# Optimization experiments

Hardware: AMD Instinct MI355X
Metric: run time of the kernel (lower is better)

## Reference

```python
import jax, jax.numpy as jnp
import numpy as np

HIDDEN = 64
EXPAND = 2
INNER = HIDDEN * EXPAND
KSIZE = 4


def setup_inputs() -> dict:
    key = jax.random.key(0)
    ks = jax.random.split(key, 12)
    s = 0.02
    inp = {
        "x": jax.random.normal(ks[0], (4, 64, 1024, HIDDEN), jnp.float32),
        "w_in": jax.random.normal(ks[1], (HIDDEN, 2 * INNER), jnp.float32) * s,
        "b_in": jnp.zeros((2 * INNER,), jnp.float32),
        "w_conv": jax.random.normal(ks[2], (INNER, 1, KSIZE), jnp.float32) * s,  # depthwise: [C,1,K]
        "b_conv": jnp.zeros((INNER,), jnp.float32),
        "w_delta": jax.random.normal(ks[3], (INNER, INNER), jnp.float32) * s,
        "b_delta": jnp.zeros((INNER,), jnp.float32),
        "w_si": jax.random.normal(ks[4], (INNER, INNER), jnp.float32) * s,
        "b_si": jnp.zeros((INNER,), jnp.float32),
        "w_so": jax.random.normal(ks[5], (INNER, INNER), jnp.float32) * s,
        "b_so": jnp.zeros((INNER,), jnp.float32),
        "a_log": jnp.zeros((INNER,), jnp.float32),   # nn.Parameter(torch.zeros)
        "d_skip": jnp.ones((INNER,), jnp.float32),   # nn.Parameter(torch.ones)
        "w_out": jax.random.normal(ks[6], (INNER, HIDDEN), jnp.float32) * s,
        "b_out": jnp.zeros((HIDDEN,), jnp.float32),
    }
    return inp


def _forward(x, w_in, b_in, w_conv, b_conv, w_delta, b_delta, w_si, b_si,
             w_so, b_so, a_log, d_skip, w_out, b_out):
    B, T, N, H = x.shape
    # [B,T,N,H] -> [B*N, T, H]
    xr = jnp.transpose(x, (0, 2, 1, 3)).reshape(B * N, T, H)
    proj = xr @ w_in + b_in                      # [BN, T, 2*inner]
    signal, gate = jnp.split(proj, 2, axis=-1)
    # causal depthwise conv1d (pad left K-1, crop to T == torch pad=K-1 then [:T])
    sc = jnp.transpose(signal, (0, 2, 1))        # [BN, inner, T]
    sc = jax.lax.conv_general_dilated(
        sc, w_conv, window_strides=(1,), padding=[(KSIZE - 1, 0)],
        dimension_numbers=("NCH", "OIH", "NCH"), feature_group_count=INNER)
    sc = sc + b_conv[None, :, None]
    signal = jax.nn.silu(jnp.transpose(sc, (0, 2, 1)))  # [BN, T, inner]
    # selective scan
    delta = jax.nn.softplus(signal @ w_delta + b_delta)
    s_in = jnp.tanh(signal @ w_si + b_si)
    s_out = jnp.tanh(signal @ w_so + b_so)
    a = -jax.nn.softplus(a_log)                  # [inner]
    decay = jnp.exp(delta * a)                   # [BN, T, inner]

    def step(state, xs):
        dec_t, si_t, so_t, sg_t = xs
        state = dec_t * state + si_t * sg_t
        return state, so_t * state + d_skip * sg_t

    # time-major for scan: [T, BN, inner]
    tm = lambda t: jnp.transpose(t, (1, 0, 2))
    init = jnp.zeros((B * N, INNER), x.dtype)
    _, hidden = jax.lax.scan(step, init, (tm(decay), tm(s_in), tm(s_out), tm(signal)))
    hidden = jnp.transpose(hidden, (1, 0, 2))    # [BN, T, inner]
    hidden = hidden * jax.nn.sigmoid(gate)
    out = hidden @ w_out + b_out                 # [BN, T, H]
    return jnp.transpose(out.reshape(B, N, T, H), (0, 2, 1, 3))


def reference(x, w_in, b_in, w_conv, b_conv, w_delta, b_delta, w_si, b_si,
              w_so, b_so, a_log, d_skip, w_out, b_out):
    return _forward(x, w_in, b_in, w_conv, b_conv, w_delta, b_delta, w_si, b_si,
                    w_so, b_so, a_log, d_skip, w_out, b_out)
```

## Files before the change

kernel.cpp:

```cpp
#include <hip/hip_runtime.h>
#include <math.h>


typedef __bf16 bf16x8 __attribute__((ext_vector_type(8)));
typedef float f32x4 __attribute__((ext_vector_type(4)));

#define LOG2E 1.44269504088896f

#define WIN_E 0
#define WD_E 16384
#define WSI_E 32768
#define WSO_E 49152
#define WOT_E 65536
#define WQ_END 73728
#define AS_BYTE (WQ_END * 2)

__device__ inline float sig_poly(float x) {
  float t = x * x;
  float u = fmaf(t, 1.f / 480.f, -1.f / 48.f);
  u = fmaf(t, u, 0.25f);
  return fmaf(x, u, 0.5f);
}
__device__ inline float tanh_poly(float z) {
  float t = z * z;
  return z * fmaf(t, fmaf(t, 2.f / 15.f, -1.f / 3.f), 1.f);
}

__device__ inline int frag_off(int col, int k, int nct) {
  int ks = k >> 5, lgk = (k >> 3) & 3, j = k & 7;
  return ((ks * nct + (col >> 4)) * 64 + ((col & 15) + (lgk << 4))) * 8 + j;
}

__global__ __launch_bounds__(256) void prep_kernel(
    const float* __restrict__ w_in, const float* __restrict__ w_delta,
    const float* __restrict__ w_si, const float* __restrict__ w_so,
    const float* __restrict__ w_out, const float* __restrict__ a_log,
    __bf16* __restrict__ wq, float* __restrict__ a_s) {
  int i = blockIdx.x * 256 + threadIdx.x;
  if (i < 16384) {
    int col = i & 255, k = i >> 8;
    wq[WIN_E + frag_off(col, k, 16)] = (__bf16)w_in[k * 256 + col];
  } else if (i < 32768) {
    int j = i - 16384, col = j & 127, k = j >> 7;
    wq[WD_E + frag_off(col, k, 8)] = (__bf16)w_delta[k * 128 + col];
  } else if (i < 49152) {
    int j = i - 32768, col = j & 127, k = j >> 7;
    wq[WSI_E + frag_off(col, k, 8)] = (__bf16)w_si[k * 128 + col];
  } else if (i < 65536) {
    int j = i - 49152, col = j & 127, k = j >> 7;
    wq[WSO_E + frag_off(col, k, 8)] = (__bf16)w_so[k * 128 + col];
  } else if (i < 73728) {
    int j = i - 65536, col = j & 63, k = j >> 6;
    wq[WOT_E + frag_off(col, k, 4)] = (__bf16)w_out[k * 64 + col];
  } else if (i < 73856) {
    int c = i - 73728;
    a_s[c] = -log1pf(__expf(a_log[c]));
  }
}

__global__ __launch_bounds__(256, 3) void mamba_main(
    const float* __restrict__ x, const float* __restrict__ b_in,
    const float* __restrict__ w_conv, const float* __restrict__ b_conv,
    const float* __restrict__ b_delta, const float* __restrict__ b_si,
    const float* __restrict__ b_so, const float* __restrict__ d_skip,
    const float* __restrict__ b_out, const __bf16* __restrict__ wqb,
    const float* __restrict__ a_s, float* __restrict__ out) {
  __shared__ __bf16 XS[32 * 72];
  __shared__ __bf16 DH[32 * 136];
  __shared__ __bf16 HG[32 * 136];

  const int tid = threadIdx.x;
  const int lane = tid & 63;
  const int wave = tid >> 6;
  const int lr = lane & 15;
  const int lg = lane >> 4;
  const int lk = lg << 3;
  const int bb = blockIdx.x >> 10;
  const int nn = blockIdx.x & 1023;

  float bsig[2], bgat[2], bdl[2], aC[2], aH[2], aQ[2], bsi[2], bso[2], dskv[2], cbc[2];
  float cw0[2], cw1[2], cw2[2], cw3[2];
#pragma unroll
  for (int ct = 0; ct < 2; ++ct) {
    int sc = wave * 32 + ct * 16 + lr;
    bsig[ct] = b_in[sc];
    bgat[ct] = b_in[128 + sc];
    bdl[ct] = b_delta[sc];
    float a = a_s[sc];
    aC[ct] = a;
    aH[ct] = 0.5f * LOG2E * a;
    aQ[ct] = 0.125f * LOG2E * a;
    bsi[ct] = b_si[sc];
    bso[ct] = b_so[sc];
    dskv[ct] = d_skip[sc];
    cw0[ct] = w_conv[sc * 4 + 0];
    cw1[ct] = w_conv[sc * 4 + 1];
    cw2[ct] = w_conv[sc * 4 + 2];
    cw3[ct] = w_conv[sc * 4 + 3];
    cbc[ct] = b_conv[sc];
  }
  const float bout = b_out[wave * 16 + lr];

  float car1[2] = {0.f, 0.f}, car2[2] = {0.f, 0.f}, car3[2] = {0.f, 0.f};
  float C[2] = {0.f, 0.f};
  float sgv[2][2][4];
  float sigg[2][2][4];

  const int xtr = tid >> 3, xc0 = (tid & 7) * 8;
  {
    const float* xp = x + (((size_t)bb * 64 + xtr) * 1024 + nn) * 64 + xc0;
    float4 v0 = *(const float4*)xp;
    float4 v1 = *(const float4*)(xp + 4);
    bf16x8 pk;
    pk[0] = (__bf16)v0.x; pk[1] = (__bf16)v0.y; pk[2] = (__bf16)v0.z; pk[3] = (__bf16)v0.w;
    pk[4] = (__bf16)v1.x; pk[5] = (__bf16)v1.y; pk[6] = (__bf16)v1.z; pk[7] = (__bf16)v1.w;
    *(bf16x8*)(XS + xtr * 72 + xc0) = pk;
  }
  __syncthreads();

#pragma unroll
  for (int ch = 0; ch < 2; ++ch) {
    const int cbs[4] = {2 * wave, 2 * wave + 1, 8 + 2 * wave, 9 + 2 * wave};
    bf16x8 bw[4][2];
#pragma unroll
    for (int ct = 0; ct < 4; ++ct)
#pragma unroll
      for (int ks = 0; ks < 2; ++ks)
        bw[ct][ks] = *(const bf16x8*)(wqb + WIN_E + (((ks << 4) + cbs[ct]) * 64 + lane) * 8);
    float4 xv0, xv1;
    if (ch == 0) {
      const float* xp = x + (((size_t)bb * 64 + 32 + xtr) * 1024 + nn) * 64 + xc0;
      xv0 = *(const float4*)xp;
      xv1 = *(const float4*)(xp + 4);
    }
    bf16x8 ax[2][2];
#pragma unroll
    for (int mt = 0; mt < 2; ++mt)
#pragma unroll
      for (int ks = 0; ks < 2; ++ks)
        ax[mt][ks] = *(const bf16x8*)(XS + (mt * 16 + lr) * 72 + ks * 32 + lk);
    f32x4 acc[2][4];
    const f32x4 z = {0.f, 0.f, 0.f, 0.f};
#pragma unroll
    for (int mt = 0; mt < 2; ++mt)
#pragma unroll
      for (int ct = 0; ct < 4; ++ct) acc[mt][ct] = z;
#pragma unroll
    for (int ks = 0; ks < 2; ++ks)
#pragma unroll
      for (int ct = 0; ct < 4; ++ct)
#pragma unroll
        for (int mt = 0; mt < 2; ++mt)
          acc[mt][ct] = __builtin_amdgcn_mfma_f32_16x16x32_bf16(ax[mt][ks], bw[ct][ks],
                                                                acc[mt][ct], 0, 0, 0);
#pragma unroll
    for (int ct = 0; ct < 2; ++ct)
#pragma unroll
      for (int mt = 0; mt < 2; ++mt)
#pragma unroll
        for (int r = 0; r < 4; ++r)
          sigg[ct][mt][r] = sig_poly(acc[mt][ct + 2][r] + bgat[ct]);
#pragma unroll
    for (int ct = 0; ct < 2; ++ct) {
      int col = wave * 32 + ct * 16 + lr;
      float s0 = acc[0][ct][0] + bsig[ct], s1 = acc[0][ct][1] + bsig[ct];
      float s2 = acc[0][ct][2] + bsig[ct], s3 = acc[0][ct][3] + bsig[ct];
      float t0 = acc[1][ct][0] + bsig[ct], t1 = acc[1][ct][1] + bsig[ct];
      float t2 = acc[1][ct][2] + bsig[ct], t3 = acc[1][ct][3] + bsig[ct];
      float a3 = __shfl_up(s3, 16), a2 = __shfl_up(s2, 16), a1 = __shfl_up(s1, 16);
      float p1 = lg ? a3 : car1[ct];
      float p2 = lg ? a2 : car2[ct];
      float p3 = lg ? a1 : car3[ct];
      float b3 = __shfl_up(t3, 16), b2 = __shfl_up(t2, 16), b1 = __shfl_up(t1, 16);
      float q15 = __shfl(s3, lr + 48), q14 = __shfl(s2, lr + 48), q13 = __shfl(s1, lr + 48);
      float e1 = lg ? b3 : q15;
      float e2 = lg ? b2 : q14;
      float e3 = lg ? b1 : q13;
      car1[ct] = __shfl(t3, lr + 48);
      car2[ct] = __shfl(t2, lr + 48);
      car3[ct] = __shfl(t1, lr + 48);
      float cv[4], dv[4];
      cv[0] = fmaf(cw0[ct], p3, fmaf(cw1[ct], p2, fmaf(cw2[ct], p1, fmaf(cw3[ct], s0, cbc[ct]))));
      cv[1] = fmaf(cw0[ct], p2, fmaf(cw1[ct], p1, fmaf(cw2[ct], s0, fmaf(cw3[ct], s1, cbc[ct]))));
      cv[2] = fmaf(cw0[ct], p1, fmaf(cw1[ct], s0, fmaf(cw2[ct], s1, fmaf(cw3[ct], s2, cbc[ct]))));
      cv[3] = fmaf(cw0[ct], s0, fmaf(cw1[ct], s1, fmaf(cw2[ct], s2, fmaf(cw3[ct], s3, cbc[ct]))));
      dv[0] = fmaf(cw0[ct], e3, fmaf(cw1[ct], e2, fmaf(cw2[ct], e1, fmaf(cw3[ct], t0, cbc[ct]))));
      dv[1] = fmaf(cw0[ct], e2, fmaf(cw1[ct], e1, fmaf(cw2[ct], t0, fmaf(cw3[ct], t1, cbc[ct]))));
      dv[2] = fmaf(cw0[ct], e1, fmaf(cw1[ct], t0, fmaf(cw2[ct], t1, fmaf(cw3[ct], t2, cbc[ct]))));
      dv[3] = fmaf(cw0[ct], t0, fmaf(cw1[ct], t1, fmaf(cw2[ct], t2, fmaf(cw3[ct], t3, cbc[ct]))));
#pragma unroll
      for (int r = 0; r < 4; ++r) {
        float c = cv[r], d = dv[r];
        float vc = c * sig_poly(c);
        float vd = d * sig_poly(d);
        sgv[ct][0][r] = vc;
        sgv[ct][1][r] = vd;
        DH[(lg * 4 + r) * 136 + col] = (__bf16)vc;
        DH[(16 + lg * 4 + r) * 136 + col] = (__bf16)vd;
      }
    }
    __syncthreads();

    bf16x8 af[2][4];
#pragma unroll
    for (int mt = 0; mt < 2; ++mt)
#pragma unroll
      for (int ks = 0; ks < 4; ++ks)
        af[mt][ks] = *(const bf16x8*)(DH + (mt * 16 + lr) * 136 + ks * 32 + lk);
    if (ch == 0) {
      bf16x8 pk;
      pk[0] = (__bf16)xv0.x; pk[1] = (__bf16)xv0.y; pk[2] = (__bf16)xv0.z; pk[3] = (__bf16)xv0.w;
      pk[4] = (__bf16)xv1.x; pk[5] = (__bf16)xv1.y; pk[6] = (__bf16)xv1.z; pk[7] = (__bf16)xv1.w;
      *(bf16x8*)(XS + xtr * 72 + xc0) = pk;
    }
#pragma unroll
    for (int ct = 0; ct < 2; ++ct) {
      const int col = wave * 32 + ct * 16 + lr;
      const int cb = 2 * wave + ct;
      const f32x4 zz = {0.f, 0.f, 0.f, 0.f};
      bf16x8 bfr[4];
#pragma unroll
      for (int ks = 0; ks < 4; ++ks)
        bfr[ks] = *(const bf16x8*)(wqb + WD_E + (((ks << 3) + cb) * 64 + lane) * 8);
      f32x4 ad[2] = {zz, zz};
#pragma unroll
      for (int ks = 0; ks < 4; ++ks)
#pragma unroll
        for (int mt = 0; mt < 2; ++mt)
          ad[mt] = __builtin_amdgcn_mfma_f32_16x16x32_bf16(af[mt][ks], bfr[ks], ad[mt], 0, 0, 0);
      float dec[2][4];
#pragma unroll
      for (int mt = 0; mt < 2; ++mt)
#pragma unroll
        for (int r = 0; r < 4; ++r) {
          float xd = ad[mt][r] + bdl[ct];
          float t = xd * xd;
          dec[mt][r] = __builtin_amdgcn_exp2f(fmaf(t, aQ[ct], fmaf(xd, aH[ct], aC[ct])));
        }
#pragma unroll
      for (int ks = 0; ks < 4; ++ks)
        bfr[ks] = *(const bf16x8*)(wqb + WSI_E + (((ks << 3) + cb) * 64 + lane) * 8);
      f32x4 as_[2] = {zz, zz};
#pragma unroll
      for (int ks = 0; ks < 4; ++ks)
#pragma unroll
        for (int mt = 0; mt < 2; ++mt)
          as_[mt] = __builtin_amdgcn_mfma_f32_16x16x32_bf16(af[mt][ks], bfr[ks], as_[mt], 0, 0, 0);
      float u[2][4];
#pragma unroll
      for (int mt = 0; mt < 2; ++mt)
#pragma unroll
        for (int r = 0; r < 4; ++r)
          u[mt][r] = tanh_poly(as_[mt][r] + bsi[ct]) * sgv[ct][mt][r];
      float p0 = u[0][0];
      float p1s = fmaf(dec[0][1], p0, u[0][1]);
      float p2s = fmaf(dec[0][2], p1s, u[0][2]);
      float p3s = fmaf(dec[0][3], p2s, u[0][3]);
      float Q0 = dec[0][0], Q1 = Q0 * dec[0][1], Q2 = Q1 * dec[0][2], Q3 = Q2 * dec[0][3];
      float r0 = u[1][0];
      float r1s = fmaf(dec[1][1], r0, u[1][1]);
      float r2s = fmaf(dec[1][2], r1s, u[1][2]);
      float r3s = fmaf(dec[1][3], r2s, u[1][3]);
      float S0 = dec[1][0], S1 = S0 * dec[1][1], S2 = S1 * dec[1][2], S3 = S2 * dec[1][3];
#pragma unroll
      for (int ks = 0; ks < 4; ++ks)
        bfr[ks] = *(const bf16x8*)(wqb + WSO_E + (((ks << 3) + cb) * 64 + lane) * 8);
      f32x4 ao[2] = {zz, zz};
#pragma unroll
      for (int ks = 0; ks < 4; ++ks)
#pragma unroll
        for (int mt = 0; mt < 2; ++mt)
          ao[mt] = __builtin_amdgcn_mfma_f32_16x16x32_bf16(af[mt][ks], bfr[ks], ao[mt], 0, 0, 0);
      float tao[2][4];
#pragma unroll
      for (int mt = 0; mt < 2; ++mt)
#pragma unroll
        for (int r = 0; r < 4; ++r) tao[mt][r] = tanh_poly(ao[mt][r] + bso[ct]);
      float Pa = Q3, La = p3s;
      float shp = __shfl_up(Pa, 16), shl = __shfl_up(La, 16);
      float Pa1 = (lg >= 1) ? Pa * shp : Pa;
      float La1 = (lg >= 1) ? fmaf(Pa, shl, La) : La;
      shp = __shfl_up(Pa1, 32); shl = __shfl_up(La1, 32);
      float Pa2 = (lg >= 2) ? Pa1 * shp : Pa1;
      float La2 = (lg >= 2) ? fmaf(Pa1, shl, La1) : La1;
      shp = __shfl_up(Pa2, 16); shl = __shfl_up(La2, 16);
      float Sin0 = lg ? fmaf(shp, C[ct], shl) : C[ct];
      float Pb = __shfl(Pa2, lr + 48), Lb = __shfl(La2, lr + 48);
      float T0 = fmaf(Pb, C[ct], Lb);
      float Pc = S3, Lc = r3s;
      shp = __shfl_up(Pc, 16); shl = __shfl_up(Lc, 16);
      float Pc1 = (lg >= 1) ? Pc * shp : Pc;
      float Lc1 = (lg >= 1) ? fmaf(Pc, shl, Lc) : Lc;
      shp = __shfl_up(Pc1, 32); shl = __shfl_up(Lc1, 32);
      float Pc2 = (lg >= 2) ? Pc1 * shp : Pc1;
      float Lc2 = (lg >= 2) ? fmaf(Pc1, shl, Lc1) : Lc1;
      shp = __shfl_up(Pc2, 16); shl = __shfl_up(Lc2, 16);
      float Sin1 = lg ? fmaf(shp, T0, shl) : T0;
      float Pd = __shfl(Pc2, lr + 48), Ld = __shfl(Lc2, lr + 48);
      C[ct] = fmaf(Pd, T0, Ld);
      float stv[2][4];
      stv[0][0] = fmaf(Q0, Sin0, p0);
      stv[0][1] = fmaf(Q1, Sin0, p1s);
      stv[0][2] = fmaf(Q2, Sin0, p2s);
      stv[0][3] = fmaf(Q3, Sin0, p3s);
      stv[1][0] = fmaf(S0, Sin1, r0);
      stv[1][1] = fmaf(S1, Sin1, r1s);
      stv[1][2] = fmaf(S2, Sin1, r2s);
      stv[1][3] = fmaf(S3, Sin1, r3s);
#pragma unroll
      for (int mt = 0; mt < 2; ++mt)
#pragma unroll
        for (int r = 0; r < 4; ++r) {
          int row = mt * 16 + lg * 4 + r;
          float h = sigg[ct][mt][r] *
                    fmaf(tao[mt][r], stv[mt][r], dskv[ct] * sgv[ct][mt][r]);
          HG[row * 136 + col] = (__bf16)h;
        }
    }
    bf16x8 bw5[4];
#pragma unroll
    for (int ks = 0; ks < 4; ++ks)
      bw5[ks] = *(const bf16x8*)(wqb + WOT_E + (((ks << 2) + wave) * 64 + lane) * 8);
    __syncthreads();

    {
      bf16x8 ah[2][4];
#pragma unroll
      for (int mt = 0; mt < 2; ++mt)
#pragma unroll
        for (int ks = 0; ks < 4; ++ks)
          ah[mt][ks] = *(const bf16x8*)(HG + (mt * 16 + lr) * 136 + ks * 32 + lk);
      const f32x4 zz = {0.f, 0.f, 0.f, 0.f};
      f32x4 a5[2] = {zz, zz};
#pragma unroll
      for (int ks = 0; ks < 4; ++ks)
#pragma unroll
        for (int mt = 0; mt < 2; ++mt)
          a5[mt] = __builtin_amdgcn_mfma_f32_16x16x32_bf16(ah[mt][ks], bw5[ks], a5[mt], 0, 0, 0);
      size_t ob = (((size_t)bb * 64 + ch * 32) * 1024 + nn) * 64 + wave * 16 + lr;
#pragma unroll
      for (int mt = 0; mt < 2; ++mt)
#pragma unroll
        for (int r = 0; r < 4; ++r)
          out[ob + (size_t)(mt * 16 + lg * 4 + r) * 65536] = a5[mt][r] + bout;
    }
  }
}

extern "C" void kernel_launch(void* const* d_in, const int* in_sizes, int n_in,
                              void* d_out, int out_size, void* d_ws, size_t ws_size,
                              hipStream_t stream) {
  const float* x = (const float*)d_in[0];
  const float* w_in = (const float*)d_in[1];
  const float* b_in = (const float*)d_in[2];
  const float* w_conv = (const float*)d_in[3];
  const float* b_conv = (const float*)d_in[4];
  const float* w_delta = (const float*)d_in[5];
  const float* b_delta = (const float*)d_in[6];
  const float* w_si = (const float*)d_in[7];
  const float* b_si = (const float*)d_in[8];
  const float* w_so = (const float*)d_in[9];
  const float* b_so = (const float*)d_in[10];
  const float* a_log = (const float*)d_in[11];
  const float* d_skip = (const float*)d_in[12];
  const float* w_out = (const float*)d_in[13];
  const float* b_out = (const float*)d_in[14];

  __bf16* wq = (__bf16*)d_ws;
  float* a_s = (float*)((char*)d_ws + AS_BYTE);

  hipLaunchKernelGGL(prep_kernel, dim3(289), dim3(256), 0, stream,
                     w_in, w_delta, w_si, w_so, w_out, a_log, wq, a_s);
  hipLaunchKernelGGL(mamba_main, dim3(4096), dim3(256), 0, stream,
                     x, b_in, w_conv, b_conv, b_delta, b_si, b_so, d_skip, b_out,
                     wq, a_s, (float*)d_out);
}
```

Before: 99.30 us.

## Loop each block over all four batches and stage output through LDS

The grid shrinks from 4096 to 1024 blocks, and each block now walks all four batch entries for one node in a non-unrolled loop. This amortizes the per-block parameter and bias loads, and lets the x prefetch run on into the next batch's first chunk. Outputs are written into a new shared-memory tile and then stored as coalesced float4 rows instead of scattered scalar stores. The delta and s_in weight fragments are also loaded together up front. In exchange there are fewer blocks to hide latency and fill the GPU, an extra barrier per chunk, and more LDS per block, which may reduce occupancy.

New measurement: 285.2 us. +187.3%, slower.

```diff
diff --git a/kernel.cpp b/kernel.cpp
--- a/kernel.cpp
+++ b/kernel.cpp
@@ -68,6 +68,7 @@
   __shared__ __bf16 XS[32 * 72];
   __shared__ __bf16 DH[32 * 136];
   __shared__ __bf16 HG[32 * 136];
+  __shared__ float OB[32 * 68];
 
   const int tid = threadIdx.x;
   const int lane = tid & 63;
@@ -75,8 +76,7 @@
   const int lr = lane & 15;
   const int lg = lane >> 4;
   const int lk = lg << 3;
-  const int bb = blockIdx.x >> 10;
-  const int nn = blockIdx.x & 1023;
+  const int nn = blockIdx.x;
 
   float bsig[2], bgat[2], bdl[2], aC[2], aH[2], aQ[2], bsi[2], bso[2], dskv[2], cbc[2];
   float cw0[2], cw1[2], cw2[2], cw3[2];
@@ -100,15 +100,11 @@
     cbc[ct] = b_conv[sc];
   }
   const float bout = b_out[wave * 16 + lr];
-
-  float car1[2] = {0.f, 0.f}, car2[2] = {0.f, 0.f}, car3[2] = {0.f, 0.f};
-  float C[2] = {0.f, 0.f};
-  float sgv[2][2][4];
-  float sigg[2][2][4];
-
   const int xtr = tid >> 3, xc0 = (tid & 7) * 8;
+  const int orow = tid >> 3, oc0 = (tid & 7) * 8;
+
   {
-    const float* xp = x + (((size_t)bb * 64 + xtr) * 1024 + nn) * 64 + xc0;
+    const float* xp = x + (((size_t)xtr * 1024 + nn) * 64) + xc0;
     float4 v0 = *(const float4*)xp;
     float4 v1 = *(const float4*)(xp + 4);
     bf16x8 pk;
@@ -118,231 +114,251 @@
   }
   __syncthreads();
 
-#pragma unroll
-  for (int ch = 0; ch < 2; ++ch) {
-    const int cbs[4] = {2 * wave, 2 * wave + 1, 8 + 2 * wave, 9 + 2 * wave};
-    bf16x8 bw[4][2];
-#pragma unroll
-    for (int ct = 0; ct < 4; ++ct)
+#pragma unroll 1
+  for (int s = 0; s < 4; ++s) {
+    float car1[2] = {0.f, 0.f}, car2[2] = {0.f, 0.f}, car3[2] = {0.f, 0.f};
+    float C[2] = {0.f, 0.f};
+    float sgv[2][2][4];
+    float sigg[2][2][4];
+
+#pragma unroll
+    for (int ch = 0; ch < 2; ++ch) {
+      const int cbs[4] = {2 * wave, 2 * wave + 1, 8 + 2 * wave, 9 + 2 * wave};
+      bf16x8 bw[4][2];
+#pragma unroll
+      for (int ct = 0; ct < 4; ++ct)
+#pragma unroll
+        for (int ks = 0; ks < 2; ++ks)
+          bw[ct][ks] = *(const bf16x8*)(wqb + WIN_E + (((ks << 4) + cbs[ct]) * 64 + lane) * 8);
+      const bool pf = (ch == 0) || (s < 3);
+      float4 xv0, xv1;
+      if (pf) {
+        int prow = s * 64 + 32 + 32 * ch + xtr;
+        const float* xp = x + (((size_t)prow * 1024 + nn) * 64) + xc0;
+        xv0 = *(const float4*)xp;
+        xv1 = *(const float4*)(xp + 4);
+      }
+      bf16x8 ax[2][2];
+#pragma unroll
+      for (int mt = 0; mt < 2; ++mt)
+#pragma unroll
+        for (int ks = 0; ks < 2; ++ks)
+          ax[mt][ks] = *(const bf16x8*)(XS + (mt * 16 + lr) * 72 + ks * 32 + lk);
+      f32x4 acc[2][4];
+      const f32x4 z = {0.f, 0.f, 0.f, 0.f};
+#pragma unroll
+      for (int mt = 0; mt < 2; ++mt)
+#pragma unroll
+        for (int ct = 0; ct < 4; ++ct) acc[mt][ct] = z;
 #pragma unroll
       for (int ks = 0; ks < 2; ++ks)
-        bw[ct][ks] = *(const bf16x8*)(wqb + WIN_E + (((ks << 4) + cbs[ct]) * 64 + lane) * 8);
-    float4 xv0, xv1;
-    if (ch == 0) {
-      const float* xp = x + (((size_t)bb * 64 + 32 + xtr) * 1024 + nn) * 64 + xc0;
-      xv0 = *(const float4*)xp;
-      xv1 = *(const float4*)(xp + 4);
-    }
-    bf16x8 ax[2][2];
-#pragma unroll
-    for (int mt = 0; mt < 2; ++mt)
-#pragma unroll
-      for (int ks = 0; ks < 2; ++ks)
-        ax[mt][ks] = *(const bf16x8*)(XS + (mt * 16 + lr) * 72 + ks * 32 + lk);
-    f32x4 acc[2][4];
-    const f32x4 z = {0.f, 0.f, 0.f, 0.f};
-#pragma unroll
-    for (int mt = 0; mt < 2; ++mt)
-#pragma unroll
-      for (int ct = 0; ct < 4; ++ct) acc[mt][ct] = z;
-#pragma unroll
-    for (int ks = 0; ks < 2; ++ks)
-#pragma unroll
-      for (int ct = 0; ct < 4; ++ct)
-#pragma unroll
-        for (int mt = 0; mt < 2; ++mt)
-          acc[mt][ct] = __builtin_amdgcn_mfma_f32_16x16x32_bf16(ax[mt][ks], bw[ct][ks],
-                                                                acc[mt][ct], 0, 0, 0);
-#pragma unroll
-    for (int ct = 0; ct < 2; ++ct)
+#pragma unroll
+        for (int ct = 0; ct < 4; ++ct)
+#pragma unroll
+          for (int mt = 0; mt < 2; ++mt)
+            acc[mt][ct] = __builtin_amdgcn_mfma_f32_16x16x32_bf16(ax[mt][ks], bw[ct][ks],
+                                                                  acc[mt][ct], 0, 0, 0);
+#pragma unroll
+      for (int ct = 0; ct < 2; ++ct)
+#pragma unroll
+        for (int mt = 0; mt < 2; ++mt)
+#pragma unroll
+          for (int r = 0; r < 4; ++r)
+            sigg[ct][mt][r] = sig_poly(acc[mt][ct + 2][r] + bgat[ct]);
+#pragma unroll
+      for (int ct = 0; ct < 2; ++ct) {
+        int col = wave * 32 + ct * 16 + lr;
+        float s0 = acc[0][ct][0] + bsig[ct], s1 = acc[0][ct][1] + bsig[ct];
+        float s2 = acc[0][ct][2] + bsig[ct], s3 = acc[0][ct][3] + bsig[ct];
+        float t0 = acc[1][ct][0] + bsig[ct], t1 = acc[1][ct][1] + bsig[ct];
+        float t2 = acc[1][ct][2] + bsig[ct], t3 = acc[1][ct][3] + bsig[ct];
+        float a3 = __shfl_up(s3, 16), a2 = __shfl_up(s2, 16), a1 = __shfl_up(s1, 16);
+        float p1 = lg ? a3 : car1[ct];
+        float p2 = lg ? a2 : car2[ct];
+        float p3 = lg ? a1 : car3[ct];
+        float b3 = __shfl_up(t3, 16), b2 = __shfl_up(t2, 16), b1 = __shfl_up(t1, 16);
+        float q15 = __shfl(s3, lr + 48), q14 = __shfl(s2, lr + 48), q13 = __shfl(s1, lr + 48);
+        float e1 = lg ? b3 : q15;
+        float e2 = lg ? b2 : q14;
+        float e3 = lg ? b1 : q13;
+        car1[ct] = __shfl(t3, lr + 48);
+        car2[ct] = __shfl(t2, lr + 48);
+        car3[ct] = __shfl(t1, lr + 48);
+        float cv[4], dv[4];
+        cv[0] = fmaf(cw0[ct], p3, fmaf(cw1[ct], p2, fmaf(cw2[ct], p1, fmaf(cw3[ct], s0, cbc[ct]))));
+        cv[1] = fmaf(cw0[ct], p2, fmaf(cw1[ct], p1, fmaf(cw2[ct], s0, fmaf(cw3[ct], s1, cbc[ct]))));
+        cv[2] = fmaf(cw0[ct], p1, fmaf(cw1[ct], s0, fmaf(cw2[ct], s1, fmaf(cw3[ct], s2, cbc[ct]))));
+        cv[3] = fmaf(cw0[ct], s0, fmaf(cw1[ct], s1, fmaf(cw2[ct], s2, fmaf(cw3[ct], s3, cbc[ct]))));
+        dv[0] = fmaf(cw0[ct], e3, fmaf(cw1[ct], e2, fmaf(cw2[ct], e1, fmaf(cw3[ct], t0, cbc[ct]))));
+        dv[1] = fmaf(cw0[ct], e2, fmaf(cw1[ct], e1, fmaf(cw2[ct], t0, fmaf(cw3[ct], t1, cbc[ct]))));
+        dv[2] = fmaf(cw0[ct], e1, fmaf(cw1[ct], t0, fmaf(cw2[ct], t1, fmaf(cw3[ct], t2, cbc[ct]))));
+        dv[3] = fmaf(cw0[ct], t0, fmaf(cw1[ct], t1, fmaf(cw2[ct], t2, fmaf(cw3[ct], t3, cbc[ct]))));
+#pragma unroll
+        for (int r = 0; r < 4; ++r) {
+          float c = cv[r], d = dv[r];
+          float vc = c * sig_poly(c);
+          float vd = d * sig_poly(d);
+          sgv[ct][0][r] = vc;
+          sgv[ct][1][r] = vd;
+          DH[(lg * 4 + r) * 136 + col] = (__bf16)vc;
+          DH[(16 + lg * 4 + r) * 136 + col] = (__bf16)vd;
+        }
+      }
+      __syncthreads();
+
+      bf16x8 af[2][4];
 #pragma unroll
       for (int mt = 0; mt < 2; ++mt)
 #pragma unroll
-        for (int r = 0; r < 4; ++r)
-          sigg[ct][mt][r] = sig_poly(acc[mt][ct + 2][r] + bgat[ct]);
-#pragma unroll
-    for (int ct = 0; ct < 2; ++ct) {
-      int col = wave * 32 + ct * 16 + lr;
-      float s0 = acc[0][ct][0] + bsig[ct], s1 = acc[0][ct][1] + bsig[ct];
-      float s2 = acc[0][ct][2] + bsig[ct], s3 = acc[0][ct][3] + bsig[ct];
-      float t0 = acc[1][ct][0] + bsig[ct], t1 = acc[1][ct][1] + bsig[ct];
-      float t2 = acc[1][ct][2] + bsig[ct], t3 = acc[1][ct][3] + bsig[ct];
-      float a3 = __shfl_up(s3, 16), a2 = __shfl_up(s2, 16), a1 = __shfl_up(s1, 16);
-      float p1 = lg ? a3 : car1[ct];
-      float p2 = lg ? a2 : car2[ct];
-      float p3 = lg ? a1 : car3[ct];
-      float b3 = __shfl_up(t3, 16), b2 = __shfl_up(t2, 16), b1 = __shfl_up(t1, 16);
-      float q15 = __shfl(s3, lr + 48), q14 = __shfl(s2, lr + 48), q13 = __shfl(s1, lr + 48);
-      float e1 = lg ? b3 : q15;
-      float e2 = lg ? b2 : q14;
-      float e3 = lg ? b1 : q13;
-      car1[ct] = __shfl(t3, lr + 48);
-      car2[ct] = __shfl(t2, lr + 48);
-      car3[ct] = __shfl(t1, lr + 48);
-      float cv[4], dv[4];
-      cv[0] = fmaf(cw0[ct], p3, fmaf(cw1[ct], p2, fmaf(cw2[ct], p1, fmaf(cw3[ct], s0, cbc[ct]))));
-      cv[1] = fmaf(cw0[ct], p2, fmaf(cw1[ct], p1, fmaf(cw2[ct], s0, fmaf(cw3[ct], s1, cbc[ct]))));
-      cv[2] = fmaf(cw0[ct], p1, fmaf(cw1[ct], s0, fmaf(cw2[ct], s1, fmaf(cw3[ct], s2, cbc[ct]))));
-      cv[3] = fmaf(cw0[ct], s0, fmaf(cw1[ct], s1, fmaf(cw2[ct], s2, fmaf(cw3[ct], s3, cbc[ct]))));
-      dv[0] = fmaf(cw0[ct], e3, fmaf(cw1[ct], e2, fmaf(cw2[ct], e1, fmaf(cw3[ct], t0, cbc[ct]))));
-      dv[1] = fmaf(cw0[ct], e2, fmaf(cw1[ct], e1, fmaf(cw2[ct], t0, fmaf(cw3[ct], t1, cbc[ct]))));
-      dv[2] = fmaf(cw0[ct], e1, fmaf(cw1[ct], t0, fmaf(cw2[ct], t1, fmaf(cw3[ct], t2, cbc[ct]))));
-      dv[3] = fmaf(cw0[ct], t0, fmaf(cw1[ct], t1, fmaf(cw2[ct], t2, fmaf(cw3[ct], t3, cbc[ct]))));
-#pragma unroll
-      for (int r = 0; r < 4; ++r) {
-        float c = cv[r], d = dv[r];
-        float vc = c * sig_poly(c);
-        float vd = d * sig_poly(d);
-        sgv[ct][0][r] = vc;
-        sgv[ct][1][r] = vd;
-        DH[(lg * 4 + r) * 136 + col] = (__bf16)vc;
-        DH[(16 + lg * 4 + r) * 136 + col] = (__bf16)vd;
-      }
-    }
-    __syncthreads();
-
-    bf16x8 af[2][4];
-#pragma unroll
-    for (int mt = 0; mt < 2; ++mt)
+        for (int ks = 0; ks < 4; ++ks)
+          af[mt][ks] = *(const bf16x8*)(DH + (mt * 16 + lr) * 136 + ks * 32 + lk);
+      if (pf) {
+        bf16x8 pk;
+        pk[0] = (__bf16)xv0.x; pk[1] = (__bf16)xv0.y; pk[2] = (__bf16)xv0.z; pk[3] = (__bf16)xv0.w;
+        pk[4] = (__bf16)xv1.x; pk[5] = (__bf16)xv1.y; pk[6] = (__bf16)xv1.z; pk[7] = (__bf16)xv1.w;
+        *(bf16x8*)(XS + xtr * 72 + xc0) = pk;
+      }
+#pragma unroll
+      for (int ct = 0; ct < 2; ++ct) {
+        const int col = wave * 32 + ct * 16 + lr;
+        const int cb = 2 * wave + ct;
+        const f32x4 zz = {0.f, 0.f, 0.f, 0.f};
+        bf16x8 bfrA[4], bfrB[4];
+#pragma unroll
+        for (int ks = 0; ks < 4; ++ks)
+          bfrA[ks] = *(const bf16x8*)(wqb + WD_E + (((ks << 3) + cb) * 64 + lane) * 8);
+#pragma unroll
+        for (int ks = 0; ks < 4; ++ks)
+          bfrB[ks] = *(const bf16x8*)(wqb + WSI_E + (((ks << 3) + cb) * 64 + lane) * 8);
+        f32x4 ad[2] = {zz, zz};
+#pragma unroll
+        for (int ks = 0; ks < 4; ++ks)
+#pragma unroll
+          for (int mt = 0; mt < 2; ++mt)
+            ad[mt] = __builtin_amdgcn_mfma_f32_16x16x32_bf16(af[mt][ks], bfrA[ks], ad[mt], 0, 0, 0);
+#pragma unroll
+        for (int ks = 0; ks < 4; ++ks)
+          bfrA[ks] = *(const bf16x8*)(wqb + WSO_E + (((ks << 3) + cb) * 64 + lane) * 8);
+        float dec[2][4];
+#pragma unroll
+        for (int mt = 0; mt < 2; ++mt)
+#pragma unroll
+          for (int r = 0; r < 4; ++r) {
+            float xd = ad[mt][r] + bdl[ct];
+            float t = xd * xd;
+            dec[mt][r] = __builtin_amdgcn_exp2f(fmaf(t, aQ[ct], fmaf(xd, aH[ct], aC[ct])));
+          }
+        f32x4 as_[2] = {zz, zz};
+#pragma unroll
+        for (int ks = 0; ks < 4; ++ks)
+#pragma unroll
+          for (int mt = 0; mt < 2; ++mt)
+            as_[mt] = __builtin_amdgcn_mfma_f32_16x16x32_bf16(af[mt][ks], bfrB[ks], as_[mt], 0, 0, 0);
+        float u[2][4];
+#pragma unroll
+        for (int mt = 0; mt < 2; ++mt)
+#pragma unroll
+          for (int r = 0; r < 4; ++r)
+            u[mt][r] = tanh_poly(as_[mt][r] + bsi[ct]) * sgv[ct][mt][r];
+        float p0 = u[0][0];
+        float p1s = fmaf(dec[0][1], p0, u[0][1]);
+        float p2s = fmaf(dec[0][2], p1s, u[0][2]);
+        float p3s = fmaf(dec[0][3], p2s, u[0][3]);
+        float Q0 = dec[0][0], Q1 = Q0 * dec[0][1], Q2 = Q1 * dec[0][2], Q3 = Q2 * dec[0][3];
+        float r0 = u[1][0];
+        float r1s = fmaf(dec[1][1], r0, u[1][1]);
+        float r2s = fmaf(dec[1][2], r1s, u[1][2]);
+        float r3s = fmaf(dec[1][3], r2s, u[1][3]);
+        float S0 = dec[1][0], S1 = S0 * dec[1][1], S2 = S1 * dec[1][2], S3 = S2 * dec[1][3];
+        f32x4 ao[2] = {zz, zz};
+#pragma unroll
+        for (int ks = 0; ks < 4; ++ks)
+#pragma unroll
+          for (int mt = 0; mt < 2; ++mt)
+            ao[mt] = __builtin_amdgcn_mfma_f32_16x16x32_bf16(af[mt][ks], bfrA[ks], ao[mt], 0, 0, 0);
+        float tao[2][4];
+#pragma unroll
+        for (int mt = 0; mt < 2; ++mt)
+#pragma unroll
+          for (int r = 0; r < 4; ++r) tao[mt][r] = tanh_poly(ao[mt][r] + bso[ct]);
+        float Pa = Q3, La = p3s;
+        float shp = __shfl_up(Pa, 16), shl = __shfl_up(La, 16);
+        float Pa1 = (lg >= 1) ? Pa * shp : Pa;
+        float La1 = (lg >= 1) ? fmaf(Pa, shl, La) : La;
+        shp = __shfl_up(Pa1, 32); shl = __shfl_up(La1, 32);
+        float Pa2 = (lg >= 2) ? Pa1 * shp : Pa1;
+        float La2 = (lg >= 2) ? fmaf(Pa1, shl, La1) : La1;
+        shp = __shfl_up(Pa2, 16); shl = __shfl_up(La2, 16);
+        float Sin0 = lg ? fmaf(shp, C[ct], shl) : C[ct];
+        float Pb = __shfl(Pa2, lr + 48), Lb = __shfl(La2, lr + 48);
+        float T0 = fmaf(Pb, C[ct], Lb);
+        float Pc = S3, Lc = r3s;
+        shp = __shfl_up(Pc, 16); shl = __shfl_up(Lc, 16);
+        float Pc1 = (lg >= 1) ? Pc * shp : Pc;
+        float Lc1 = (lg >= 1) ? fmaf(Pc, shl, Lc) : Lc;
+        shp = __shfl_up(Pc1, 32); shl = __shfl_up(Lc1, 32);
+        float Pc2 = (lg >= 2) ? Pc1 * shp : Pc1;
+        float Lc2 = (lg >= 2) ? fmaf(Pc1, shl, Lc1) : Lc1;
+        shp = __shfl_up(Pc2, 16); shl = __shfl_up(Lc2, 16);
+        float Sin1 = lg ? fmaf(shp, T0, shl) : T0;
+        float Pd = __shfl(Pc2, lr + 48), Ld = __shfl(Lc2, lr + 48);
+        C[ct] = fmaf(Pd, T0, Ld);
+        float stv[2][4];
+        stv[0][0] = fmaf(Q0, Sin0, p0);
+        stv[0][1] = fmaf(Q1, Sin0, p1s);
+        stv[0][2] = fmaf(Q2, Sin0, p2s);
+        stv[0][3] = fmaf(Q3, Sin0, p3s);
+        stv[1][0] = fmaf(S0, Sin1, r0);
+        stv[1][1] = fmaf(S1, Sin1, r1s);
+        stv[1][2] = fmaf(S2, Sin1, r2s);
+        stv[1][3] = fmaf(S3, Sin1, r3s);
+#pragma unroll
+        for (int mt = 0; mt < 2; ++mt)
+#pragma unroll
+          for (int r = 0; r < 4; ++r) {
+            int row = mt * 16 + lg * 4 + r;
+            float h = sigg[ct][mt][r] *
+                      fmaf(tao[mt][r], stv[mt][r], dskv[ct] * sgv[ct][mt][r]);
+            HG[row * 136 + col] = (__bf16)h;
+          }
+      }
+      bf16x8 bw5[4];
 #pragma unroll
       for (int ks = 0; ks < 4; ++ks)
-        af[mt][ks] = *(const bf16x8*)(DH + (mt * 16 + lr) * 136 + ks * 32 + lk);
-    if (ch == 0) {
-      bf16x8 pk;
-      pk[0] = (__bf16)xv0.x; pk[1] = (__bf16)xv0.y; pk[2] = (__bf16)xv0.z; pk[3] = (__bf16)xv0.w;
-      pk[4] = (__bf16)xv1.x; pk[5] = (__bf16)xv1.y; pk[6] = (__bf16)xv1.z; pk[7] = (__bf16)xv1.w;
-      *(bf16x8*)(XS + xtr * 72 + xc0) = pk;
-    }
-#pragma unroll
-    for (int ct = 0; ct < 2; ++ct) {
-      const int col = wave * 32 + ct * 16 + lr;
-      const int cb = 2 * wave + ct;
-      const f32x4 zz = {0.f, 0.f, 0.f, 0.f};
-      bf16x8 bfr[4];
-#pragma unroll
-      for (int ks = 0; ks < 4; ++ks)
-        bfr[ks] = *(const bf16x8*)(wqb + WD_E + (((ks << 3) + cb) * 64 + lane) * 8);
-      f32x4 ad[2] = {zz, zz};
-#pragma unroll
-      for (int ks = 0; ks < 4; ++ks)
-#pragma unroll
-        for (int mt = 0; mt < 2; ++mt)
-          ad[mt] = __builtin_amdgcn_mfma_f32_16x16x32_bf16(af[mt][ks], bfr[ks], ad[mt], 0, 0, 0);
-      float dec[2][4];
-#pragma unroll
-      for (int mt = 0; mt < 2; ++mt)
-#pragma unroll
-        for (int r = 0; r < 4; ++r) {
-          float xd = ad[mt][r] + bdl[ct];
-          float t = xd * xd;
-          dec[mt][r] = __builtin_amdgcn_exp2f(fmaf(t, aQ[ct], fmaf(xd, aH[ct], aC[ct])));
-        }
-#pragma unroll
-      for (int ks = 0; ks < 4; ++ks)
-        bfr[ks] = *(const bf16x8*)(wqb + WSI_E + (((ks << 3) + cb) * 64 + lane) * 8);
-      f32x4 as_[2] = {zz, zz};
-#pragma unroll
-      for (int ks = 0; ks < 4; ++ks)
-#pragma unroll
-        for (int mt = 0; mt < 2; ++mt)
-          as_[mt] = __builtin_amdgcn_mfma_f32_16x16x32_bf16(af[mt][ks], bfr[ks], as_[mt], 0, 0, 0);
-      float u[2][4];
-#pragma unroll
-      for (int mt = 0; mt < 2; ++mt)
-#pragma unroll
-        for (int r = 0; r < 4; ++r)
-          u[mt][r] = tanh_poly(as_[mt][r] + bsi[ct]) * sgv[ct][mt][r];
-      float p0 = u[0][0];
-      float p1s = fmaf(dec[0][1], p0, u[0][1]);
-      float p2s = fmaf(dec[0][2], p1s, u[0][2]);
-      float p3s = fmaf(dec[0][3], p2s, u[0][3]);
-      float Q0 = dec[0][0], Q1 = Q0 * dec[0][1], Q2 = Q1 * dec[0][2], Q3 = Q2 * dec[0][3];
-      float r0 = u[1][0];
-      float r1s = fmaf(dec[1][1], r0, u[1][1]);
-      float r2s = fmaf(dec[1][2], r1s, u[1][2]);
-      float r3s = fmaf(dec[1][3], r2s, u[1][3]);
-      float S0 = dec[1][0], S1 = S0 * dec[1][1], S2 = S1 * dec[1][2], S3 = S2 * dec[1][3];
-#pragma unroll
-      for (int ks = 0; ks < 4; ++ks)
-        bfr[ks] = *(const bf16x8*)(wqb + WSO_E + (((ks << 3) + cb) * 64 + lane) * 8);
-      f32x4 ao[2] = {zz, zz};
-#pragma unroll
-      for (int ks = 0; ks < 4; ++ks)
-#pragma unroll
-        for (int mt = 0; mt < 2; ++mt)
-          ao[mt] = __builtin_amdgcn_mfma_f32_16x16x32_bf16(af[mt][ks], bfr[ks], ao[mt], 0, 0, 0);
-      float tao[2][4];
-#pragma unroll
-      for (int mt = 0; mt < 2; ++mt)
-#pragma unroll
-        for (int r = 0; r < 4; ++r) tao[mt][r] = tanh_poly(ao[mt][r] + bso[ct]);
-      float Pa = Q3, La = p3s;
-      float shp = __shfl_up(Pa, 16), shl = __shfl_up(La, 16);
-      float Pa1 = (lg >= 1) ? Pa * shp : Pa;
-      float La1 = (lg >= 1) ? fmaf(Pa, shl, La) : La;
-      shp = __shfl_up(Pa1, 32); shl = __shfl_up(La1, 32);
-      float Pa2 = (lg >= 2) ? Pa1 * shp : Pa1;
-      float La2 = (lg >= 2) ? fmaf(Pa1, shl, La1) : La1;
-      shp = __shfl_up(Pa2, 16); shl = __shfl_up(La2, 16);
-      float Sin0 = lg ? fmaf(shp, C[ct], shl) : C[ct];
-      float Pb = __shfl(Pa2, lr + 48), Lb = __shfl(La2, lr + 48);
-      float T0 = fmaf(Pb, C[ct], Lb);
-      float Pc = S3, Lc = r3s;
-      shp = __shfl_up(Pc, 16); shl = __shfl_up(Lc, 16);
-      float Pc1 = (lg >= 1) ? Pc * shp : Pc;
-      float Lc1 = (lg >= 1) ? fmaf(Pc, shl, Lc) : Lc;
-      shp = __shfl_up(Pc1, 32); shl = __shfl_up(Lc1, 32);
-      float Pc2 = (lg >= 2) ? Pc1 * shp : Pc1;
-      float Lc2 = (lg >= 2) ? fmaf(Pc1, shl, Lc1) : Lc1;
-      shp = __shfl_up(Pc2, 16); shl = __shfl_up(Lc2, 16);
-      float Sin1 = lg ? fmaf(shp, T0, shl) : T0;
-      float Pd = __shfl(Pc2, lr + 48), Ld = __shfl(Lc2, lr + 48);
-      C[ct] = fmaf(Pd, T0, Ld);
-      float stv[2][4];
-      stv[0][0] = fmaf(Q0, Sin0, p0);
-      stv[0][1] = fmaf(Q1, Sin0, p1s);
-      stv[0][2] = fmaf(Q2, Sin0, p2s);
-      stv[0][3] = fmaf(Q3, Sin0, p3s);
-      stv[1][0] = fmaf(S0, Sin1, r0);
-      stv[1][1] = fmaf(S1, Sin1, r1s);
-      stv[1][2] = fmaf(S2, Sin1, r2s);
-      stv[1][3] = fmaf(S3, Sin1, r3s);
-#pragma unroll
-      for (int mt = 0; mt < 2; ++mt)
-#pragma unroll
-        for (int r = 0; r < 4; ++r) {
-          int row = mt * 16 + lg * 4 + r;
-          float h = sigg[ct][mt][r] *
-                    fmaf(tao[mt][r], stv[mt][r], dskv[ct] * sgv[ct][mt][r]);
-          HG[row * 136 + col] = (__bf16)h;
-        }
-    }
-    bf16x8 bw5[4];
-#pragma unroll
-    for (int ks = 0; ks < 4; ++ks)
-      bw5[ks] = *(const bf16x8*)(wqb + WOT_E + (((ks << 2) + wave) * 64 + lane) * 8);
-    __syncthreads();
-
-    {
-      bf16x8 ah[2][4];
-#pragma unroll
-      for (int mt = 0; mt < 2; ++mt)
-#pragma unroll
-        for (int ks = 0; ks < 4; ++ks)
-          ah[mt][ks] = *(const bf16x8*)(HG + (mt * 16 + lr) * 136 + ks * 32 + lk);
-      const f32x4 zz = {0.f, 0.f, 0.f, 0.f};
-      f32x4 a5[2] = {zz, zz};
-#pragma unroll
-      for (int ks = 0; ks < 4; ++ks)
-#pragma unroll
-        for (int mt = 0; mt < 2; ++mt)
-          a5[mt] = __builtin_amdgcn_mfma_f32_16x16x32_bf16(ah[mt][ks], bw5[ks], a5[mt], 0, 0, 0);
-      size_t ob = (((size_t)bb * 64 + ch * 32) * 1024 + nn) * 64 + wave * 16 + lr;
-#pragma unroll
-      for (int mt = 0; mt < 2; ++mt)
-#pragma unroll
-        for (int r = 0; r < 4; ++r)
-          out[ob + (size_t)(mt * 16 + lg * 4 + r) * 65536] = a5[mt][r] + bout;
+        bw5[ks] = *(const bf16x8*)(wqb + WOT_E + (((ks << 2) + wave) * 64 + lane) * 8);
+      __syncthreads();
+
+      {
+        bf16x8 ah[2][4];
+#pragma unroll
+        for (int mt = 0; mt < 2; ++mt)
+#pragma unroll
+          for (int ks = 0; ks < 4; ++ks)
+            ah[mt][ks] = *(const bf16x8*)(HG + (mt * 16 + lr) * 136 + ks * 32 + lk);
+        const f32x4 zz = {0.f, 0.f, 0.f, 0.f};
+        f32x4 a5[2] = {zz, zz};
+#pragma unroll
+        for (int ks = 0; ks < 4; ++ks)
+#pragma unroll
+          for (int mt = 0; mt < 2; ++mt)
+            a5[mt] = __builtin_amdgcn_mfma_f32_16x16x32_bf16(ah[mt][ks], bw5[ks], a5[mt], 0, 0, 0);
+        int hcol = wave * 16 + lr;
+#pragma unroll
+        for (int mt = 0; mt < 2; ++mt)
+#pragma unroll
+          for (int r = 0; r < 4; ++r)
+            OB[(mt * 16 + lg * 4 + r) * 68 + hcol] = a5[mt][r] + bout;
+      }
+      __syncthreads();
+
+      {
+        const float* ob = OB + orow * 68 + oc0;
+        float4 v0 = *(const float4*)ob;
+        float4 v1 = *(const float4*)(ob + 4);
+        float* op = out + (((size_t)(s * 64 + ch * 32 + orow) * 1024 + nn) * 64) + oc0;
+        *(float4*)op = v0;
+        *(float4*)(op + 4) = v1;
+      }
     }
   }
 }
@@ -371,7 +387,7 @@
 
   hipLaunchKernelGGL(prep_kernel, dim3(289), dim3(256), 0, stream,
                      w_in, w_delta, w_si, w_so, w_out, a_log, wq, a_s);
-  hipLaunchKernelGGL(mamba_main, dim3(4096), dim3(256), 0, stream,
+  hipLaunchKernelGGL(mamba_main, dim3(1024), dim3(256), 0, stream,
                      x, b_in, w_conv, b_conv, b_delta, b_si, b_so, d_skip, b_out,
                      wq, a_s, (float*)d_out);
 }
```
